# Kernel tuning notes

Hardware: AMD Instinct MI355X
Metric: run time of the kernel (lower is better)

The kernel has to match this reference:

```python
import jax, jax.numpy as jnp
import numpy as np

B, E, T = 8192, 512, 32


def setup_inputs() -> dict:
    key = jax.random.key(0)
    k1, k2, k3, k4, k5, k6 = jax.random.split(key, 6)
    s1 = 1.0 / np.sqrt(E)  # torch nn.Linear default init scale (uniform bound)
    return {
        "g_exp": jax.random.normal(k1, (B, E), dtype=jnp.float32),
        "tissue_vector": jax.random.randint(k2, (B, 1), 0, T, dtype=jnp.int64),
        # per-tissue head params: Linear(E,E) then Linear(E,1)
        "W1": jax.random.uniform(k3, (T, E, E), jnp.float32, -s1, s1),
        "b1": jax.random.uniform(k4, (T, E), jnp.float32, -s1, s1),
        "W2": jax.random.uniform(k5, (T, E), jnp.float32, -s1, s1),
        "b2": jax.random.uniform(k6, (T,), jnp.float32, -s1, s1),
    }


def reference(g_exp, tissue_vector, W1, b1, W2, b2):
    # Each sample b is routed through the MLP head of its tissue id.
    # Vectorized: run every sample through every tissue head, then select.
    # h[b,t,:] = GELU(g_exp[b] @ W1[t] + b1[t])
    h = jax.nn.gelu(jnp.einsum("be,teh->bth", g_exp, W1) + b1[None, :, :],
                    approximate=False)  # exact erf GELU, matches torch nn.GELU
    # y[b,t] = softplus(h[b,t] @ W2[t] + b2[t])   (Softplus since loss_fn='poisson')
    y = jax.nn.softplus(jnp.einsum("bth,th->bt", h, W2) + b2[None, :])
    tid = tissue_vector[:, 0]  # [B], tissue id per sample
    return jnp.take_along_axis(y, tid[:, None], axis=1)  # [B, 1]
```

## Files before the change

kernel.cpp:

```cpp
#include <hip/hip_runtime.h>
#include <hip/hip_bf16.h>
#include <math.h>

#define B_N 8192
#define E_N 512
#define T_N 32
#define BP 520

typedef short bf16x8 __attribute__((ext_vector_type(8)));
typedef float f32x4 __attribute__((ext_vector_type(4)));

#define WS_OFFS   256
#define WS_RANK   512
#define WS_ORDER  33280
#define WS_YACC   66048
#define WS_YACC8  98816
#define WS_REQ    (WS_YACC8 + 8 * B_N * 4)

typedef __attribute__((address_space(1))) const unsigned int gas_u32;
typedef __attribute__((address_space(3))) unsigned int las_u32;

static __device__ __forceinline__ unsigned short f2bf(float f) {
    unsigned int u = __float_as_uint(f);
    unsigned int r = u + 0x7fffu + ((u >> 16) & 1u);
    return (unsigned short)(r >> 16);
}

static __device__ __forceinline__ unsigned int pk2(float a, float b) {
    __hip_bfloat162 h = __float22bfloat162_rn(float2{a, b});
    unsigned int u;
    __builtin_memcpy(&u, &h, 4);
    return u;
}

__global__ __launch_bounds__(512, 1) void k_gemm_mfma(
    const float* __restrict__ g_exp, const float* __restrict__ W1,
    const int* __restrict__ tv, const float* __restrict__ b1,
    const float* __restrict__ W2, float* __restrict__ yacc8) {
    int wi = blockIdx.x;
    int t = wi & 31, nt = wi >> 5;
    int n0 = nt * 64;

    int tid = threadIdx.x;
    int w = tid >> 6, lane = tid & 63;
    int quad = (lane >> 4) & 3, l15 = lane & 15;

    __shared__ __align__(16) unsigned short Bs[64 * BP];
    __shared__ __align__(16) float As[3][128 * 32];
    __shared__ int rows_s[512];
    __shared__ int wsum[8];

    float b1v[4], w2v[4];
#pragma unroll
    for (int ni = 0; ni < 4; ++ni) {
        int n = t * E_N + n0 + ni * 16 + l15;
        b1v[ni] = b1[n];
        w2v[ni] = W2[n];
    }

    int tvals[16];
    const int4* tvp = (const int4*)(tv + tid * 16);
#pragma unroll
    for (int j = 0; j < 4; ++j) ((int4*)tvals)[j] = tvp[j];
    int myc = 0;
#pragma unroll
    for (int j = 0; j < 16; ++j) myc += (tvals[j] == t) ? 1 : 0;
    int inc = myc;
#pragma unroll
    for (int o = 1; o < 64; o <<= 1) {
        int u = __shfl_up(inc, o, 64);
        if (lane >= o) inc += u;
    }
    if (lane == 63) wsum[w] = inc;
    rows_s[tid] = 0;
    __syncthreads();
    int n_t = 0, wbase = 0;
#pragma unroll
    for (int i = 0; i < 8; ++i) {
        int v = wsum[i];
        n_t += v;
        if (i < w) wbase += v;
    }
    int nt_c = n_t > 512 ? 512 : n_t;
    int rk = wbase + inc - myc;
#pragma unroll
    for (int j = 0; j < 16; ++j)
        if (tvals[j] == t) {
            int rr = rk++;
            if (rr < 512) rows_s[rr] = tid * 16 + j;
        }

    const float* Wsrc = W1 + (size_t)t * E_N * E_N + n0;
    unsigned int* Bw = (unsigned int*)Bs;
#pragma unroll
    for (int i = 0; i < 8; ++i) {
        int flat = i * 512 + tid;
        int k2 = flat >> 4, nq = flat & 15;
        float4 va = *(const float4*)(Wsrc + (size_t)(2 * k2) * E_N + nq * 4);
        float4 vb = *(const float4*)(Wsrc + (size_t)(2 * k2 + 1) * E_N + nq * 4);
        Bw[(nq * 4 + 0) * 260 + k2] = pk2(va.x, vb.x);
        Bw[(nq * 4 + 1) * 260 + k2] = pk2(va.y, vb.y);
        Bw[(nq * 4 + 2) * 260 + k2] = pk2(va.z, vb.z);
        Bw[(nq * 4 + 3) * 260 + k2] = pk2(va.w, vb.w);
    }
    __syncthreads();

    int d0 = tid, d1 = tid + 512;
    int ar0 = d0 >> 3, ac0 = (d0 & 7) ^ (ar0 & 7);
    int ar1 = d1 >> 3, ac1 = (d1 & 7) ^ (ar1 & 7);

    int lrow = w * 16 + l15;
    int c0 = (quad * 2) ^ (lrow & 7);
    int c1 = (quad * 2 + 1) ^ (lrow & 7);

    float* slab = yacc8 + (size_t)nt * B_N;

    int MC = (nt_c + 127) >> 7;
    for (int mc = 0; mc < MC; ++mc) {
        const float* pA0 = g_exp + (size_t)rows_s[mc * 128 + ar0] * E_N + ac0 * 4;
        const float* pA1 = g_exp + (size_t)rows_s[mc * 128 + ar1] * E_N + ac1 * 4;

#define ISSUE(kk) do {                                                                      \
        __builtin_amdgcn_global_load_lds((gas_u32*)(pA0 + (kk) * 32),                       \
                                         (las_u32*)&As[(kk) % 3][d0 * 4], 16, 0, 0);        \
        __builtin_amdgcn_global_load_lds((gas_u32*)(pA1 + (kk) * 32),                       \
                                         (las_u32*)&As[(kk) % 3][d1 * 4], 16, 0, 0);        \
    } while (0)

        ISSUE(0);
        ISSUE(1);

        f32x4 acc[4];
#pragma unroll
        for (int ni = 0; ni < 4; ++ni) acc[ni] = (f32x4){0.f, 0.f, 0.f, 0.f};

#define STAGE(it, W) do {                                                                   \
        asm volatile("s_waitcnt vmcnt(%0)" :: "n"(W) : "memory");                           \
        asm volatile("s_barrier" ::: "memory");                                             \
        const float* Ab = &As[(it) % 3][0];                                                 \
        f32x4 lo = *(const f32x4*)(Ab + (lrow * 8 + c0) * 4);                               \
        f32x4 hi = *(const f32x4*)(Ab + (lrow * 8 + c1) * 4);                               \
        unsigned int uu[4] = {pk2(lo[0], lo[1]), pk2(lo[2], lo[3]),                         \
                              pk2(hi[0], hi[1]), pk2(hi[2], hi[3])};                        \
        bf16x8 af;                                                                          \
        __builtin_memcpy(&af, uu, 16);                                                      \
        _Pragma("unroll") for (int ni = 0; ni < 4; ++ni) {                                  \
            bf16x8 bfr = *(const bf16x8*)(Bs + (ni * 16 + l15) * BP + (it) * 32 + quad * 8);\
            acc[ni] = __builtin_amdgcn_mfma_f32_16x16x32_bf16(af, bfr, acc[ni], 0, 0, 0);   \
        }                                                                                   \
        if ((it) + 2 < 16) ISSUE((it) + 2);                                                 \
    } while (0)

        STAGE(0, 2);  STAGE(1, 2);  STAGE(2, 2);  STAGE(3, 2);
        STAGE(4, 2);  STAGE(5, 2);  STAGE(6, 2);  STAGE(7, 2);
        STAGE(8, 2);  STAGE(9, 2);  STAGE(10, 2); STAGE(11, 2);
        STAGE(12, 2); STAGE(13, 2); STAGE(14, 2); STAGE(15, 0);
#undef STAGE
#undef ISSUE

        float pr[4] = {0.f, 0.f, 0.f, 0.f};
#pragma unroll
        for (int ni = 0; ni < 4; ++ni) {
#pragma unroll
            for (int r = 0; r < 4; ++r) {
                float u = acc[ni][r] + b1v[ni];
                float gg = 0.5f * u * (1.f + erff(u * 0.70710678118654752f));
                pr[r] = fmaf(gg, w2v[ni], pr[r]);
            }
        }
#pragma unroll
        for (int off = 1; off <= 8; off <<= 1)
#pragma unroll
            for (int r = 0; r < 4; ++r) pr[r] += __shfl_xor(pr[r], off, 64);

        if (l15 == 0) {
#pragma unroll
            for (int r = 0; r < 4; ++r) {
                int rr = mc * 128 + w * 16 + quad * 4 + r;
                if (rr < nt_c) slab[rows_s[rr]] = pr[r];
            }
        }
    }
}

__global__ void k_final8(const float* __restrict__ yacc8, const int* __restrict__ tv,
                         const float* __restrict__ b2, float* __restrict__ out) {
    int b = blockIdx.x * blockDim.x + threadIdx.x;
    if (b < B_N) {
        float x = b2[tv[b]];
#pragma unroll
        for (int s = 0; s < 8; ++s) x += yacc8[(size_t)s * B_N + b];
        out[b] = fmaxf(x, 0.f) + log1pf(expf(-fabsf(x)));
    }
}

__global__ __launch_bounds__(256) void k_prep_sb(
    const int* __restrict__ tv, int* __restrict__ offs_g,
    int* __restrict__ rank, int* __restrict__ order, float* __restrict__ yacc) {
    __shared__ int lh[4][32], wcur[4][32], offs_s[33];
    int tid = threadIdx.x, w = tid >> 6;
    if (tid < 128) lh[tid >> 5][tid & 31] = 0;
    __syncthreads();
    int tval[32];
#pragma unroll
    for (int c = 0; c < 32; ++c) tval[c] = tv[c * 256 + tid];
#pragma unroll
    for (int c = 0; c < 32; ++c) atomicAdd(&lh[w][tval[c]], 1);
    __syncthreads();
    if (tid < 32) {
        int s = lh[0][tid] + lh[1][tid] + lh[2][tid] + lh[3][tid];
        int excl = 0;
#pragma unroll
        for (int i = 0; i < 32; ++i) {
            int v = __shfl(s, i, 64);
            if (i < tid) excl += v;
        }
        offs_s[tid] = excl;
        offs_g[tid] = excl;
        if (tid == 31) { offs_s[32] = excl + s; offs_g[32] = excl + s; }
    }
    __syncthreads();
    if (tid < 128) {
        int ww = tid >> 5, t = tid & 31;
        int s = offs_s[t];
        for (int w2 = 0; w2 < ww; ++w2) s += lh[w2][t];
        wcur[ww][t] = s;
    }
    __syncthreads();
#pragma unroll
    for (int c = 0; c < 32; ++c) {
        int b = c * 256 + tid;
        int pos = atomicAdd(&wcur[w][tval[c]], 1);
        rank[b] = pos;
        order[pos] = b;
    }
    float4 z = make_float4(0.f, 0.f, 0.f, 0.f);
#pragma unroll
    for (int c = 0; c < 8; ++c) *(float4*)(yacc + (c * 256 + tid) * 4) = z;
}

__global__ __launch_bounds__(256) void fb_gemm(
    const float* __restrict__ g_exp, const float* __restrict__ W1,
    const float* __restrict__ b1, const float* __restrict__ W2,
    const int* __restrict__ offs, const int* __restrict__ order,
    float* __restrict__ yacc) {
    int t = blockIdx.z;
    int base = offs[t];
    int n_t = offs[t + 1] - base;
    int m0 = blockIdx.y * 64;
    if (m0 >= n_t) return;
    int n0 = blockIdx.x * 128;

    __shared__ float As2[32][68];
    __shared__ float Bs2[32][128];
    __shared__ int sidx[64];

    int tid = threadIdx.x;
    if (tid < 64) {
        int m = m0 + tid;
        sidx[tid] = (m < n_t) ? order[base + m] : -1;
    }
    __syncthreads();

    int ty = tid >> 4, tx = tid & 15;
    float acc[4][8];
#pragma unroll
    for (int r = 0; r < 4; ++r)
#pragma unroll
        for (int c = 0; c < 8; ++c) acc[r][c] = 0.f;

    for (int k0 = 0; k0 < E_N; k0 += 32) {
#pragma unroll
        for (int p = 0; p < 2; ++p) {
            int idx = tid + 256 * p;
            int row = idx >> 3, kcq = idx & 7;
            int s = sidx[row];
            float4 v = make_float4(0.f, 0.f, 0.f, 0.f);
            if (s >= 0) v = *(const float4*)(g_exp + (size_t)s * E_N + k0 + kcq * 4);
            As2[kcq * 4 + 0][row] = v.x;
            As2[kcq * 4 + 1][row] = v.y;
            As2[kcq * 4 + 2][row] = v.z;
            As2[kcq * 4 + 3][row] = v.w;
        }
#pragma unroll
        for (int p = 0; p < 4; ++p) {
            int idx = tid + 256 * p;
            int kr = idx >> 5, c4 = idx & 31;
            *(float4*)(&Bs2[kr][c4 * 4]) =
                *(const float4*)(W1 + ((size_t)t * E_N + (k0 + kr)) * E_N + n0 + c4 * 4);
        }
        __syncthreads();
#pragma unroll
        for (int e = 0; e < 32; ++e) {
            float4 a = *(const float4*)(&As2[e][ty * 4]);
            float4 bA = *(const float4*)(&Bs2[e][tx * 4]);
            float4 bB = *(const float4*)(&Bs2[e][tx * 4 + 64]);
            float av[4] = {a.x, a.y, a.z, a.w};
            float bv[8] = {bA.x, bA.y, bA.z, bA.w, bB.x, bB.y, bB.z, bB.w};
#pragma unroll
            for (int r = 0; r < 4; ++r)
#pragma unroll
                for (int c = 0; c < 8; ++c) acc[r][c] = fmaf(av[r], bv[c], acc[r][c]);
        }
        __syncthreads();
    }

    float pr[4] = {0.f, 0.f, 0.f, 0.f};
#pragma unroll
    for (int c = 0; c < 8; ++c) {
        int n = n0 + tx * 4 + ((c >= 4) ? 64 : 0) + (c & 3);
        float bb = b1[t * E_N + n];
        float w2 = W2[t * E_N + n];
#pragma unroll
        for (int r = 0; r < 4; ++r) {
            float u = acc[r][c] + bb;
            float g = 0.5f * u * (1.f + erff(u * 0.70710678118654752f));
            pr[r] = fmaf(g, w2, pr[r]);
        }
    }
#pragma unroll
    for (int off = 8; off >= 1; off >>= 1)
#pragma unroll
        for (int r = 0; r < 4; ++r) pr[r] += __shfl_xor(pr[r], off, 64);

    if (tx == 0) {
#pragma unroll
        for (int r = 0; r < 4; ++r) {
            int m = m0 + ty * 4 + r;
            if (m < n_t) atomicAdd(&yacc[sidx[ty * 4 + r]], pr[r]);
        }
    }
}

__global__ void fb_final(const float* __restrict__ yacc, const int* __restrict__ tv,
                         const float* __restrict__ b2, float* __restrict__ out) {
    int b = blockIdx.x * blockDim.x + threadIdx.x;
    if (b < B_N) {
        float x = yacc[b] + b2[tv[b]];
        out[b] = fmaxf(x, 0.f) + log1pf(expf(-fabsf(x)));
    }
}

extern "C" void kernel_launch(void* const* d_in, const int* in_sizes, int n_in,
                              void* d_out, int out_size, void* d_ws, size_t ws_size,
                              hipStream_t stream) {
    const float* g_exp = (const float*)d_in[0];
    const int*   tv    = (const int*)d_in[1];
    const float* W1    = (const float*)d_in[2];
    const float* b1    = (const float*)d_in[3];
    const float* W2    = (const float*)d_in[4];
    const float* b2    = (const float*)d_in[5];
    float* out = (float*)d_out;

    char* ws = (char*)d_ws;

    if (ws_size >= (size_t)WS_REQ) {
        float* yacc8 = (float*)(ws + WS_YACC8);
        k_gemm_mfma<<<256, 512, 0, stream>>>(g_exp, W1, tv, b1, W2, yacc8);
        k_final8<<<32, 256, 0, stream>>>(yacc8, tv, b2, out);
    } else {
        int* offs   = (int*)(ws + WS_OFFS);
        int* rank   = (int*)(ws + WS_RANK);
        int* order  = (int*)(ws + WS_ORDER);
        float* yacc = (float*)(ws + WS_YACC);
        k_prep_sb<<<1, 256, 0, stream>>>(tv, offs, rank, order, yacc);
        fb_gemm<<<dim3(4, 8, 32), 256, 0, stream>>>(g_exp, W1, b1, W2, offs, order, yacc);
        fb_final<<<32, 256, 0, stream>>>(yacc, tv, b2, out);
    }
}
```

Baseline: 114.5 us.

## Split row chunks across two blocks and load A directly from global

The grid doubles to 512 blocks, with each (tissue, n-tile) pair's 128-row chunks interleaved between two blocks, so per-block work halves and more blocks run concurrently. The LDS triple-buffered async A staging with barriers is removed; each lane now reads its A fragment straight from global memory into registers. Launch bounds rise to allow more occupancy. The trade-off is that each W1 tile is converted to bf16 twice (once per half-block), and A loads are no longer explicitly pipelined, so they rely on occupancy to hide latency.

```diff
diff --git a/kernel.cpp b/kernel.cpp
--- a/kernel.cpp
+++ b/kernel.cpp
@@ -17,9 +17,6 @@
 #define WS_YACC8  98816
 #define WS_REQ    (WS_YACC8 + 8 * B_N * 4)
 
-typedef __attribute__((address_space(1))) const unsigned int gas_u32;
-typedef __attribute__((address_space(3))) unsigned int las_u32;
-
 static __device__ __forceinline__ unsigned short f2bf(float f) {
     unsigned int u = __float_as_uint(f);
     unsigned int r = u + 0x7fffu + ((u >> 16) & 1u);
@@ -33,12 +30,12 @@
     return u;
 }
 
-__global__ __launch_bounds__(512, 1) void k_gemm_mfma(
+__global__ __launch_bounds__(512, 4) void k_gemm_mfma(
     const float* __restrict__ g_exp, const float* __restrict__ W1,
     const int* __restrict__ tv, const float* __restrict__ b1,
     const float* __restrict__ W2, float* __restrict__ yacc8) {
     int wi = blockIdx.x;
-    int t = wi & 31, nt = wi >> 5;
+    int t = wi & 31, nt = (wi >> 5) & 7, h = wi >> 8;
     int n0 = nt * 64;
 
     int tid = threadIdx.x;
@@ -46,8 +43,7 @@
     int quad = (lane >> 4) & 3, l15 = lane & 15;
 
     __shared__ __align__(16) unsigned short Bs[64 * BP];
-    __shared__ __align__(16) float As[3][128 * 32];
-    __shared__ int rows_s[512];
+    __shared__ int rows_s[256];
     __shared__ int wsum[8];
 
     float b1v[4], w2v[4];
@@ -72,7 +68,7 @@
         if (lane >= o) inc += u;
     }
     if (lane == 63) wsum[w] = inc;
-    rows_s[tid] = 0;
+    if (tid < 256) rows_s[tid] = 0;
     __syncthreads();
     int n_t = 0, wbase = 0;
 #pragma unroll
@@ -87,7 +83,8 @@
     for (int j = 0; j < 16; ++j)
         if (tvals[j] == t) {
             int rr = rk++;
-            if (rr < 512) rows_s[rr] = tid * 16 + j;
+            if (rr < 512 && (((rr >> 7) & 1) == h))
+                rows_s[((rr >> 8) << 7) | (rr & 127)] = tid * 16 + j;
         }
 
     const float* Wsrc = W1 + (size_t)t * E_N * E_N + n0;
@@ -105,58 +102,33 @@
     }
     __syncthreads();
 
-    int d0 = tid, d1 = tid + 512;
-    int ar0 = d0 >> 3, ac0 = (d0 & 7) ^ (ar0 & 7);
-    int ar1 = d1 >> 3, ac1 = (d1 & 7) ^ (ar1 & 7);
-
-    int lrow = w * 16 + l15;
-    int c0 = (quad * 2) ^ (lrow & 7);
-    int c1 = (quad * 2 + 1) ^ (lrow & 7);
+    int MCn = (nt_c + 127) >> 7;
+    int MC = (MCn + 1 - h) >> 1;
 
     float* slab = yacc8 + (size_t)nt * B_N;
 
-    int MC = (nt_c + 127) >> 7;
     for (int mc = 0; mc < MC; ++mc) {
-        const float* pA0 = g_exp + (size_t)rows_s[mc * 128 + ar0] * E_N + ac0 * 4;
-        const float* pA1 = g_exp + (size_t)rows_s[mc * 128 + ar1] * E_N + ac1 * 4;
-
-#define ISSUE(kk) do {                                                                      \
-        __builtin_amdgcn_global_load_lds((gas_u32*)(pA0 + (kk) * 32),                       \
-                                         (las_u32*)&As[(kk) % 3][d0 * 4], 16, 0, 0);        \
-        __builtin_amdgcn_global_load_lds((gas_u32*)(pA1 + (kk) * 32),                       \
-                                         (las_u32*)&As[(kk) % 3][d1 * 4], 16, 0, 0);        \
-    } while (0)
-
-        ISSUE(0);
-        ISSUE(1);
+        int row = rows_s[mc * 128 + w * 16 + l15];
+        const f32x4* pA4 = (const f32x4*)(g_exp + (size_t)row * E_N + quad * 8);
 
         f32x4 acc[4];
 #pragma unroll
         for (int ni = 0; ni < 4; ++ni) acc[ni] = (f32x4){0.f, 0.f, 0.f, 0.f};
 
-#define STAGE(it, W) do {                                                                   \
-        asm volatile("s_waitcnt vmcnt(%0)" :: "n"(W) : "memory");                           \
-        asm volatile("s_barrier" ::: "memory");                                             \
-        const float* Ab = &As[(it) % 3][0];                                                 \
-        f32x4 lo = *(const f32x4*)(Ab + (lrow * 8 + c0) * 4);                               \
-        f32x4 hi = *(const f32x4*)(Ab + (lrow * 8 + c1) * 4);                               \
-        unsigned int uu[4] = {pk2(lo[0], lo[1]), pk2(lo[2], lo[3]),                         \
-                              pk2(hi[0], hi[1]), pk2(hi[2], hi[3])};                        \
-        bf16x8 af;                                                                          \
-        __builtin_memcpy(&af, uu, 16);                                                      \
-        _Pragma("unroll") for (int ni = 0; ni < 4; ++ni) {                                  \
-            bf16x8 bfr = *(const bf16x8*)(Bs + (ni * 16 + l15) * BP + (it) * 32 + quad * 8);\
-            acc[ni] = __builtin_amdgcn_mfma_f32_16x16x32_bf16(af, bfr, acc[ni], 0, 0, 0);   \
-        }                                                                                   \
-        if ((it) + 2 < 16) ISSUE((it) + 2);                                                 \
-    } while (0)
-
-        STAGE(0, 2);  STAGE(1, 2);  STAGE(2, 2);  STAGE(3, 2);
-        STAGE(4, 2);  STAGE(5, 2);  STAGE(6, 2);  STAGE(7, 2);
-        STAGE(8, 2);  STAGE(9, 2);  STAGE(10, 2); STAGE(11, 2);
-        STAGE(12, 2); STAGE(13, 2); STAGE(14, 2); STAGE(15, 0);
-#undef STAGE
-#undef ISSUE
+#pragma unroll
+        for (int ks = 0; ks < 16; ++ks) {
+            f32x4 lo = pA4[ks * 8];
+            f32x4 hi = pA4[ks * 8 + 1];
+            unsigned int uu[4] = {pk2(lo[0], lo[1]), pk2(lo[2], lo[3]),
+                                  pk2(hi[0], hi[1]), pk2(hi[2], hi[3])};
+            bf16x8 af;
+            __builtin_memcpy(&af, uu, 16);
+#pragma unroll
+            for (int ni = 0; ni < 4; ++ni) {
+                bf16x8 bfr = *(const bf16x8*)(Bs + (ni * 16 + l15) * BP + ks * 32 + quad * 8);
+                acc[ni] = __builtin_amdgcn_mfma_f32_16x16x32_bf16(af, bfr, acc[ni], 0, 0, 0);
+            }
+        }
 
         float pr[4] = {0.f, 0.f, 0.f, 0.f};
 #pragma unroll
@@ -176,8 +148,9 @@
         if (l15 == 0) {
 #pragma unroll
             for (int r = 0; r < 4; ++r) {
-                int rr = mc * 128 + w * 16 + quad * 4 + r;
-                if (rr < nt_c) slab[rows_s[rr]] = pr[r];
+                int lidx = mc * 128 + w * 16 + quad * 4 + r;
+                int grr = (2 * mc + h) * 128 + w * 16 + quad * 4 + r;
+                if (grr < nt_c) slab[rows_s[lidx]] = pr[r];
             }
         }
     }
@@ -356,7 +329,7 @@
 
     if (ws_size >= (size_t)WS_REQ) {
         float* yacc8 = (float*)(ws + WS_YACC8);
-        k_gemm_mfma<<<256, 512, 0, stream>>>(g_exp, W1, tv, b1, W2, yacc8);
+        k_gemm_mfma<<<512, 512, 0, stream>>>(g_exp, W1, tv, b1, W2, yacc8);
         k_final8<<<32, 256, 0, stream>>>(yacc8, tv, b2, out);
     } else {
         int* offs   = (int*)(ws + WS_OFFS);
```

Measured after the change: 226.9 us. +98.0%, slower.
